# Kernel tuning notes

Measured on AMD Instinct MI355X. Metric: run time of the kernel, lower is better.

## Reference

```python
import jax, jax.numpy as jnp
import numpy as np

B, S, V, D, C = 2048, 256, 30522, 768, 100


def setup_inputs() -> dict:
    key = jax.random.key(0)
    k_ids, k_mask, k_emb, k_w1, k_b1, k_w2, k_b2 = jax.random.split(key, 7)
    input_ids = jax.random.randint(k_ids, (B, S), 0, V, dtype=jnp.int64)
    # ensure at least one valid token per row (avoid 0/0 in masked mean)
    attention_mask = jax.random.randint(k_mask, (B, S), 0, 2, dtype=jnp.int64)
    attention_mask = attention_mask.at[:, 0].set(1)
    scale = 1.0 / np.sqrt(D)
    return {
        "input_ids": input_ids,
        "attention_mask": attention_mask,
        "embed_table": jax.random.normal(k_emb, (V, D), dtype=jnp.float32) * 0.02,
        "W1": jax.random.normal(k_w1, (D, D), dtype=jnp.float32) * scale,
        "b1": jax.random.normal(k_b1, (D,), dtype=jnp.float32) * 0.01,
        "W2": jax.random.normal(k_w2, (D, C), dtype=jnp.float32) * scale,
        "b2": jax.random.normal(k_b2, (C,), dtype=jnp.float32) * 0.01,
    }


def reference(input_ids, attention_mask, embed_table, W1, b1, W2, b2):
    # Embedding lookup: [B, S, D]
    word_features = embed_table[input_ids]
    # Fused masked mean pooling over the whole batch (replaces python loop):
    # sum of valid token embeddings / count of valid tokens, per sample.
    mask = attention_mask.astype(word_features.dtype)          # [B, S]
    summed = jnp.einsum("bsd,bs->bd", word_features, mask)     # [B, D]
    counts = jnp.sum(mask, axis=1, keepdims=True)              # [B, 1]
    bow_features = summed / counts                              # [B, D]
    # 2-layer MLP head
    h = jax.nn.relu(bow_features @ W1 + b1)                     # [B, D]
    target_scores = h @ W2 + b2                                 # [B, C]
    return (target_scores, target_scores)
```

## Files before the change

### kernel.cpp

```cpp
#include <hip/hip_runtime.h>

#define B_ 2048
#define S_ 256
#define V_ 30522
#define D_ 768
#define C_ 100
#define NPAD 112

__device__ __forceinline__ unsigned short f2bf(float x) {
  unsigned u = __builtin_bit_cast(unsigned, x);
  u = (u + 0x7fffu + ((u >> 16) & 1u)) >> 16;
  return (unsigned short)u;
}

typedef __attribute__((ext_vector_type(8))) short bf16x8;
typedef __attribute__((ext_vector_type(4))) float f32x4;

__global__ __launch_bounds__(256) void prep_kernel(
    const int* __restrict__ ids, const int* __restrict__ mask,
    const float* __restrict__ w1, const float* __restrict__ w2,
    int* __restrict__ cids, int* __restrict__ cnts,
    unsigned short* __restrict__ w1t, unsigned short* __restrict__ w2t) {
  const int bid = blockIdx.x;
  const int t = threadIdx.x;
  if (bid < 512) {
    const int wv = t >> 6, lane = t & 63;
    const int b = bid * 4 + wv;
    const int base = b * S_;
    int total = 0;
#pragma unroll
    for (int r = 0; r < S_ / 64; ++r) {
      const int s = r * 64 + lane;
      const int m = mask[base + s];
      const unsigned long long bal = __ballot(m != 0);
      const int pre = __popcll(bal & ((1ull << lane) - 1ull));
      if (m) cids[base + total + pre] = ids[base + s];
      total += __popcll(bal);
    }
    if (lane == 0) cnts[b] = total;
  } else if (bid < 1088) {
    __shared__ float tile[32][33];
    const int local = bid - 512;
    const int k0 = (local % 24) * 32, n0 = (local / 24) * 32;
    const int tx = t & 31, ty = t >> 5;
#pragma unroll
    for (int i = 0; i < 4; ++i)
      tile[ty + i * 8][tx] = w1[(size_t)(k0 + ty + i * 8) * D_ + n0 + tx];
    __syncthreads();
#pragma unroll
    for (int i = 0; i < 4; ++i) {
      const int n = ty + i * 8;
      w1t[(size_t)(n0 + n) * D_ + k0 + tx] = f2bf(tile[tx][n]);
    }
  } else {
    __shared__ float tile[32][33];
    const int local = bid - 1088;
    const int k0 = (local % 24) * 32, n0 = (local / 24) * 32;
    const int tx = t & 31, ty = t >> 5;
#pragma unroll
    for (int i = 0; i < 4; ++i) {
      const int k = k0 + ty + i * 8, n = n0 + tx;
      tile[ty + i * 8][tx] = (n < C_) ? w2[(size_t)k * C_ + n] : 0.f;
    }
    __syncthreads();
#pragma unroll
    for (int i = 0; i < 4; ++i) {
      const int n = n0 + ty + i * 8;
      if (n < NPAD)
        w2t[(size_t)n * D_ + k0 + tx] = f2bf(tile[tx][ty + i * 8]);
    }
  }
}

__global__ __launch_bounds__(256) void pool_sliced(
    const int* __restrict__ cids, const int* __restrict__ cnts,
    const float* __restrict__ table, unsigned short* __restrict__ bowb) {
  __shared__ int sids[4][S_];
  const int bid = blockIdx.x;
  const int grp = bid >> 3;
  const int wv = threadIdx.x >> 6;
  const int lane = threadIdx.x & 63;
  const int sub = lane >> 3;
  const int cg = lane & 7;

  for (int pass = 0; pass < 3; ++pass) {
    const int chunk = pass * 8 + (bid & 7);
    const int coff = chunk * 32 + cg * 4;
    for (int i = 0; i < 2; ++i) {
      const int smp = grp * 8 + wv * 2 + i;
      const int cnt = cnts[smp];
      const int* cp = cids + (size_t)smp * S_;
      const int id0 = cp[0];
#pragma unroll
      for (int r = 0; r < S_ / 64; ++r) {
        const int idx = r * 64 + lane;
        sids[wv][idx] = (idx < cnt) ? cp[idx] : id0;
      }
      float a0 = 0.f, a1 = 0.f, a2 = 0.f, a3 = 0.f;
      const int nb = (cnt + 63) >> 6;
      for (int b = 0; b < nb; ++b) {
        float4 v[8];
#pragma unroll
        for (int j = 0; j < 8; ++j) {
          const int id = sids[wv][b * 64 + j * 8 + sub];
          v[j] = *reinterpret_cast<const float4*>(table + (size_t)id * D_ + coff);
        }
#pragma unroll
        for (int j = 0; j < 8; ++j) {
          a0 += v[j].x; a1 += v[j].y; a2 += v[j].z; a3 += v[j].w;
        }
      }
#pragma unroll
      for (int m = 8; m <= 32; m <<= 1) {
        a0 += __shfl_xor(a0, m);
        a1 += __shfl_xor(a1, m);
        a2 += __shfl_xor(a2, m);
        a3 += __shfl_xor(a3, m);
      }
      if (sub == 0) {
        const float fp = (float)(nb * 64 - cnt);
        const float4 v0 =
            *reinterpret_cast<const float4*>(table + (size_t)id0 * D_ + coff);
        a0 -= fp * v0.x; a1 -= fp * v0.y; a2 -= fp * v0.z; a3 -= fp * v0.w;
        const float inv = 1.0f / (float)cnt;
        ushort4 o;
        o.x = f2bf(a0 * inv); o.y = f2bf(a1 * inv);
        o.z = f2bf(a2 * inv); o.w = f2bf(a3 * inv);
        *reinterpret_cast<ushort4*>(bowb + (size_t)smp * D_ + coff) = o;
      }
    }
  }
}

#define G1_BM 32
#define G1_BN 64
#define G1_LDK 72

__global__ __launch_bounds__(256) void gemm1_mfma(
    const unsigned short* __restrict__ Ab, const unsigned short* __restrict__ Bt,
    const float* __restrict__ bias, unsigned short* __restrict__ Hb) {
  __shared__ unsigned short As[G1_BM][G1_LDK];
  __shared__ unsigned short Bs[G1_BN][G1_LDK];
  const int tid = threadIdx.x;
  const int bm = blockIdx.x * G1_BM;
  const int bn = blockIdx.y * G1_BN;
  const int w = tid >> 6;
  const int l = tid & 63;
  const int r = l & 15;
  const int g = l >> 4;

  f32x4 acc0 = {0.f, 0.f, 0.f, 0.f};
  f32x4 acc1 = {0.f, 0.f, 0.f, 0.f};

  const int ar = tid >> 3;
  const int kc8 = (tid & 7) * 8;

  for (int k0 = 0; k0 < D_; k0 += 64) {
    __syncthreads();
    *reinterpret_cast<int4*>(&As[ar][kc8]) =
        *reinterpret_cast<const int4*>(&Ab[(size_t)(bm + ar) * D_ + k0 + kc8]);
    *reinterpret_cast<int4*>(&Bs[ar][kc8]) =
        *reinterpret_cast<const int4*>(&Bt[(size_t)(bn + ar) * D_ + k0 + kc8]);
    *reinterpret_cast<int4*>(&Bs[ar + 32][kc8]) =
        *reinterpret_cast<const int4*>(&Bt[(size_t)(bn + ar + 32) * D_ + k0 + kc8]);
    __syncthreads();
    const bf16x8 a00 = *reinterpret_cast<const bf16x8*>(&As[r][g * 8]);
    const bf16x8 a01 = *reinterpret_cast<const bf16x8*>(&As[r][32 + g * 8]);
    const bf16x8 a10 = *reinterpret_cast<const bf16x8*>(&As[16 + r][g * 8]);
    const bf16x8 a11 = *reinterpret_cast<const bf16x8*>(&As[16 + r][32 + g * 8]);
    const bf16x8 b0 = *reinterpret_cast<const bf16x8*>(&Bs[w * 16 + r][g * 8]);
    const bf16x8 b1 = *reinterpret_cast<const bf16x8*>(&Bs[w * 16 + r][32 + g * 8]);
    acc0 = __builtin_amdgcn_mfma_f32_16x16x32_bf16(a00, b0, acc0, 0, 0, 0);
    acc0 = __builtin_amdgcn_mfma_f32_16x16x32_bf16(a01, b1, acc0, 0, 0, 0);
    acc1 = __builtin_amdgcn_mfma_f32_16x16x32_bf16(a10, b0, acc1, 0, 0, 0);
    acc1 = __builtin_amdgcn_mfma_f32_16x16x32_bf16(a11, b1, acc1, 0, 0, 0);
  }

  const int col = bn + w * 16 + r;
  const float bb = bias[col];
#pragma unroll
  for (int q = 0; q < 4; ++q) {
    const int row0 = bm + g * 4 + q;
    float v0 = acc0[q] + bb;
    v0 = v0 > 0.f ? v0 : 0.f;
    Hb[(size_t)row0 * D_ + col] = f2bf(v0);
    float v1 = acc1[q] + bb;
    v1 = v1 > 0.f ? v1 : 0.f;
    Hb[(size_t)(row0 + 16) * D_ + col] = f2bf(v1);
  }
}

__global__ __launch_bounds__(64) void gemm2_mfma(
    const unsigned short* __restrict__ Hb, const unsigned short* __restrict__ w2t,
    const float* __restrict__ b2, float* __restrict__ out) {
  const int bm = blockIdx.x * 16;
  const int bn = blockIdx.y * 16;
  const int l = threadIdx.x;
  const int r = l & 15;
  const int g = l >> 4;

  const unsigned short* ap = Hb + (size_t)(bm + r) * D_ + g * 8;
  const unsigned short* bp = w2t + (size_t)(bn + r) * D_ + g * 8;

  f32x4 acc = {0.f, 0.f, 0.f, 0.f};
#pragma unroll
  for (int k0 = 0; k0 < D_; k0 += 32) {
    const bf16x8 av = *reinterpret_cast<const bf16x8*>(ap + k0);
    const bf16x8 bv = *reinterpret_cast<const bf16x8*>(bp + k0);
    acc = __builtin_amdgcn_mfma_f32_16x16x32_bf16(av, bv, acc, 0, 0, 0);
  }

  const int col = bn + r;
  if (col < C_) {
    const float bb = b2[col];
#pragma unroll
    for (int q = 0; q < 4; ++q) {
      const int row = bm + g * 4 + q;
      const float v = acc[q] + bb;
      out[(size_t)row * C_ + col] = v;
      out[(size_t)row * C_ + col + (size_t)B_ * C_] = v;
    }
  }
}

extern "C" void kernel_launch(void* const* d_in, const int* in_sizes, int n_in,
                              void* d_out, int out_size, void* d_ws,
                              size_t ws_size, hipStream_t stream) {
  const int* ids = (const int*)d_in[0];
  const int* mask = (const int*)d_in[1];
  const float* table = (const float*)d_in[2];
  const float* W1 = (const float*)d_in[3];
  const float* b1 = (const float*)d_in[4];
  const float* W2 = (const float*)d_in[5];
  const float* b2 = (const float*)d_in[6];
  float* out = (float*)d_out;

  const size_t BOWB = (size_t)B_ * D_ * 2;
  const size_t HBB  = (size_t)B_ * D_ * 2;
  const size_t W1TB = (size_t)D_ * D_ * 2;
  const size_t W2TB = (size_t)NPAD * D_ * 2;
  const size_t CIDB = (size_t)B_ * S_ * 4;

  char* p = (char*)d_ws;
  unsigned short* bowb = (unsigned short*)p;
  unsigned short* hb   = (unsigned short*)(p + BOWB);
  unsigned short* w1t  = (unsigned short*)(p + BOWB + HBB);
  unsigned short* w2t  = (unsigned short*)(p + BOWB + HBB + W1TB);
  int* cids            = (int*)(p + BOWB + HBB + W1TB + W2TB);
  int* cnts            = (int*)(p + BOWB + HBB + W1TB + W2TB + CIDB);

  prep_kernel<<<1184, 256, 0, stream>>>(ids, mask, W1, W2, cids, cnts, w1t, w2t);
  pool_sliced<<<2048, 256, 0, stream>>>(cids, cnts, table, bowb);
  gemm1_mfma<<<dim3(B_ / G1_BM, D_ / G1_BN), 256, 0, stream>>>(bowb, w1t, b1, hb);
  gemm2_mfma<<<dim3(B_ / 16, NPAD / 16), 64, 0, stream>>>(hb, w2t, b2, out);
}
```

Before: 97.56 us.

## Convert embedding table to bf16 in prep and pool from bf16 copy

The prep kernel now also converts the whole fp32 embedding table to a bf16 copy in the workspace on every call. Pooling then gathers 8 bf16 values per lane from that copy, which halves the bytes read per token in the dominant gather phase. Pooling is split into two launches with 64-column chunks: the first covers 512 columns, and the second covers the remaining 256 columns with each block handling fewer samples. It also drops the padded-row subtraction in favour of per-token bounds checks. In exchange there is an extra full-table read and write each call, plus bf16 rounding of the embeddings before accumulation.

```diff
diff --git a/kernel.cpp b/kernel.cpp
--- a/kernel.cpp
+++ b/kernel.cpp
@@ -12,20 +12,37 @@
   u = (u + 0x7fffu + ((u >> 16) & 1u)) >> 16;
   return (unsigned short)u;
 }
+__device__ __forceinline__ float bf_lo(unsigned u) {
+  return __builtin_bit_cast(float, u << 16);
+}
+__device__ __forceinline__ float bf_hi(unsigned u) {
+  return __builtin_bit_cast(float, u & 0xffff0000u);
+}
 
 typedef __attribute__((ext_vector_type(8))) short bf16x8;
 typedef __attribute__((ext_vector_type(4))) float f32x4;
 
 __global__ __launch_bounds__(256) void prep_kernel(
     const int* __restrict__ ids, const int* __restrict__ mask,
-    const float* __restrict__ w1, const float* __restrict__ w2,
+    const float* __restrict__ table, const float* __restrict__ w1,
+    const float* __restrict__ w2, unsigned short* __restrict__ tbb,
     int* __restrict__ cids, int* __restrict__ cnts,
     unsigned short* __restrict__ w1t, unsigned short* __restrict__ w2t) {
   const int bid = blockIdx.x;
   const int t = threadIdx.x;
-  if (bid < 512) {
+  if (bid < 2048) {
+    const int n4 = (V_ * D_) / 4;
+    int i = bid * 256 + t;
+    const int stride = 2048 * 256;
+    for (; i < n4; i += stride) {
+      const float4 v = reinterpret_cast<const float4*>(table)[i];
+      ushort4 o;
+      o.x = f2bf(v.x); o.y = f2bf(v.y); o.z = f2bf(v.z); o.w = f2bf(v.w);
+      reinterpret_cast<ushort4*>(tbb)[i] = o;
+    }
+  } else if (bid < 2560) {
     const int wv = t >> 6, lane = t & 63;
-    const int b = bid * 4 + wv;
+    const int b = (bid - 2048) * 4 + wv;
     const int base = b * S_;
     int total = 0;
 #pragma unroll
@@ -38,9 +55,9 @@
       total += __popcll(bal);
     }
     if (lane == 0) cnts[b] = total;
-  } else if (bid < 1088) {
+  } else if (bid < 3136) {
     __shared__ float tile[32][33];
-    const int local = bid - 512;
+    const int local = bid - 2560;
     const int k0 = (local % 24) * 32, n0 = (local / 24) * 32;
     const int tx = t & 31, ty = t >> 5;
 #pragma unroll
@@ -54,7 +71,7 @@
     }
   } else {
     __shared__ float tile[32][33];
-    const int local = bid - 1088;
+    const int local = bid - 3136;
     const int k0 = (local % 24) * 32, n0 = (local / 24) * 32;
     const int tx = t & 31, ty = t >> 5;
 #pragma unroll
@@ -72,62 +89,70 @@
   }
 }
 
-__global__ __launch_bounds__(256) void pool_sliced(
+__global__ __launch_bounds__(256) void pool_bf16_sliced(
     const int* __restrict__ cids, const int* __restrict__ cnts,
-    const float* __restrict__ table, unsigned short* __restrict__ bowb) {
+    const unsigned short* __restrict__ tbb, unsigned short* __restrict__ bowb,
+    int pass) {
   __shared__ int sids[4][S_];
   const int bid = blockIdx.x;
-  const int grp = bid >> 3;
   const int wv = threadIdx.x >> 6;
   const int lane = threadIdx.x & 63;
   const int sub = lane >> 3;
   const int cg = lane & 7;
-
-  for (int pass = 0; pass < 3; ++pass) {
-    const int chunk = pass * 8 + (bid & 7);
-    const int coff = chunk * 32 + cg * 4;
-    for (int i = 0; i < 2; ++i) {
-      const int smp = grp * 8 + wv * 2 + i;
-      const int cnt = cnts[smp];
-      const int* cp = cids + (size_t)smp * S_;
-      const int id0 = cp[0];
-#pragma unroll
-      for (int r = 0; r < S_ / 64; ++r) {
-        const int idx = r * 64 + lane;
-        sids[wv][idx] = (idx < cnt) ? cp[idx] : id0;
+  int chunk, smp0, nsmp;
+  if (pass == 0) {
+    chunk = bid & 7; smp0 = (bid >> 3) * 8; nsmp = 8;
+  } else {
+    const int x = bid & 7;
+    chunk = 8 + (x >> 1);
+    smp0 = (x & 1) * (B_ / 2) + (bid >> 3) * 4;
+    nsmp = 4;
+  }
+  const int coff = chunk * 64 + cg * 8;
+
+  for (int s = wv; s < nsmp; s += 4) {
+    const int smp = smp0 + s;
+    const int cnt = cnts[smp];
+    const int* cp = cids + (size_t)smp * S_;
+#pragma unroll
+    for (int r = 0; r < S_ / 64; ++r) {
+      const int idx = r * 64 + lane;
+      sids[wv][idx] = (idx < cnt) ? cp[idx] : cp[0];
+    }
+    float a[8] = {};
+    for (int base = 0; base < cnt; base += 64) {
+      int4 v[8];
+#pragma unroll
+      for (int j = 0; j < 8; ++j) {
+        int tt = base + j * 8 + sub;
+        tt = tt < S_ ? tt : S_ - 1;
+        const int id = sids[wv][tt];
+        v[j] = *reinterpret_cast<const int4*>(tbb + (size_t)id * D_ + coff);
       }
-      float a0 = 0.f, a1 = 0.f, a2 = 0.f, a3 = 0.f;
-      const int nb = (cnt + 63) >> 6;
-      for (int b = 0; b < nb; ++b) {
-        float4 v[8];
-#pragma unroll
-        for (int j = 0; j < 8; ++j) {
-          const int id = sids[wv][b * 64 + j * 8 + sub];
-          v[j] = *reinterpret_cast<const float4*>(table + (size_t)id * D_ + coff);
-        }
-#pragma unroll
-        for (int j = 0; j < 8; ++j) {
-          a0 += v[j].x; a1 += v[j].y; a2 += v[j].z; a3 += v[j].w;
+#pragma unroll
+      for (int j = 0; j < 8; ++j) {
+        if (base + j * 8 + sub < cnt) {
+          const unsigned* u = reinterpret_cast<const unsigned*>(&v[j]);
+#pragma unroll
+          for (int q = 0; q < 4; ++q) {
+            a[2 * q]     += bf_lo(u[q]);
+            a[2 * q + 1] += bf_hi(u[q]);
+          }
         }
       }
-#pragma unroll
-      for (int m = 8; m <= 32; m <<= 1) {
-        a0 += __shfl_xor(a0, m);
-        a1 += __shfl_xor(a1, m);
-        a2 += __shfl_xor(a2, m);
-        a3 += __shfl_xor(a3, m);
-      }
-      if (sub == 0) {
-        const float fp = (float)(nb * 64 - cnt);
-        const float4 v0 =
-            *reinterpret_cast<const float4*>(table + (size_t)id0 * D_ + coff);
-        a0 -= fp * v0.x; a1 -= fp * v0.y; a2 -= fp * v0.z; a3 -= fp * v0.w;
-        const float inv = 1.0f / (float)cnt;
-        ushort4 o;
-        o.x = f2bf(a0 * inv); o.y = f2bf(a1 * inv);
-        o.z = f2bf(a2 * inv); o.w = f2bf(a3 * inv);
-        *reinterpret_cast<ushort4*>(bowb + (size_t)smp * D_ + coff) = o;
-      }
+    }
+#pragma unroll
+    for (int m = 8; m <= 32; m <<= 1) {
+#pragma unroll
+      for (int q = 0; q < 8; ++q) a[q] += __shfl_xor(a[q], m);
+    }
+    if (sub == 0) {
+      const float inv = 1.0f / (float)cnt;
+      unsigned short o[8];
+#pragma unroll
+      for (int q = 0; q < 8; ++q) o[q] = f2bf(a[q] * inv);
+      *reinterpret_cast<int4*>(bowb + (size_t)smp * D_ + coff) =
+          *reinterpret_cast<const int4*>(o);
     }
   }
 }
@@ -240,6 +265,7 @@
   const size_t W1TB = (size_t)D_ * D_ * 2;
   const size_t W2TB = (size_t)NPAD * D_ * 2;
   const size_t CIDB = (size_t)B_ * S_ * 4;
+  const size_t CNTB = (size_t)B_ * 4;
 
   char* p = (char*)d_ws;
   unsigned short* bowb = (unsigned short*)p;
@@ -248,9 +274,13 @@
   unsigned short* w2t  = (unsigned short*)(p + BOWB + HBB + W1TB);
   int* cids            = (int*)(p + BOWB + HBB + W1TB + W2TB);
   int* cnts            = (int*)(p + BOWB + HBB + W1TB + W2TB + CIDB);
-
-  prep_kernel<<<1184, 256, 0, stream>>>(ids, mask, W1, W2, cids, cnts, w1t, w2t);
-  pool_sliced<<<2048, 256, 0, stream>>>(cids, cnts, table, bowb);
+  unsigned short* tbb  =
+      (unsigned short*)(p + BOWB + HBB + W1TB + W2TB + CIDB + CNTB);
+
+  prep_kernel<<<3232, 256, 0, stream>>>(ids, mask, table, W1, W2, tbb, cids,
+                                        cnts, w1t, w2t);
+  pool_bf16_sliced<<<2048, 256, 0, stream>>>(cids, cnts, tbb, bowb, 0);
+  pool_bf16_sliced<<<2048, 256, 0, stream>>>(cids, cnts, tbb, bowb, 1);
   gemm1_mfma<<<dim3(B_ / G1_BM, D_ / G1_BN), 256, 0, stream>>>(bowb, w1t, b1, hb);
   gemm2_mfma<<<dim3(B_ / 16, NPAD / 16), 64, 0, stream>>>(hb, w2t, b2, out);
 }
```

Measured after the change: 80.12 us. 1.22x faster.
